# Optimization experiments

Measured on AMD Instinct MI355X. Metric: run time of the kernel, lower is better.

Reference implementation:

```python
import jax, jax.numpy as jnp
import numpy as np

N = 50000
E = 600000
D = 128


def gcn_conv(x, row, col, w, W, b):
    """PyG GCNConv: add self-loops (weight 1), symmetric deg^-1/2 normalization,
    linear transform, edge-weighted scatter-add aggregation, then bias."""
    n = x.shape[0]
    loop = jnp.arange(n)
    r = jnp.concatenate([row, loop])            # source nodes, [E+N]
    c = jnp.concatenate([col, loop])            # target nodes, [E+N]
    ww = jnp.concatenate([w, jnp.ones((n,), x.dtype)])
    deg = jax.ops.segment_sum(ww, c, num_segments=n)          # weighted in-degree
    dinv = jnp.where(deg > 0, jax.lax.rsqrt(deg), jnp.zeros_like(deg))
    norm = dinv[r] * ww * dinv[c]               # [E+N]
    xl = x @ W                                  # [n, D_out]
    msg = norm[:, None] * xl[r]                 # gather + scale, [E+N, D_out]
    out = jax.ops.segment_sum(msg, c, num_segments=n)
    return out + b


def setup_inputs() -> dict:
    key = jax.random.key(0)
    ks = jax.random.split(key, 12)
    x = jax.random.normal(ks[0], (N, D), dtype=jnp.float32)
    edge_index = jax.random.randint(ks[1], (2, E), 0, N, dtype=jnp.int64)
    edge_weights = jax.random.uniform(ks[2], (E,), dtype=jnp.float32)
    s = 1.0 / np.sqrt(D)
    W1 = jax.random.uniform(ks[3], (D, D), jnp.float32, -s, s)
    b1 = jnp.zeros((D,), jnp.float32)
    W2 = jax.random.uniform(ks[4], (D, D), jnp.float32, -s, s)
    b2 = jnp.zeros((D,), jnp.float32)
    W3 = jax.random.uniform(ks[5], (D, D), jnp.float32, -s, s)
    b3 = jnp.zeros((D,), jnp.float32)
    prelu_w = jnp.array(0.25, jnp.float32)
    return {"x": x, "edge_index": edge_index, "edge_weights": edge_weights,
            "W1": W1, "b1": b1, "W2": W2, "b2": b2, "W3": W3, "b3": b3,
            "prelu_w": prelu_w}


def reference(x, edge_index, edge_weights, W1, b1, W2, b2, W3, b3, prelu_w):
    row, col = edge_index[0], edge_index[1]
    # layer 1: GCNConv -> (dropout: eval, identity) -> ELU
    h = gcn_conv(x, row, col, edge_weights, W1, b1)
    h = jax.nn.elu(h)
    # layer 2: GCNConv -> GELU (torch default = exact erf)
    h = gcn_conv(h, row, col, edge_weights, W2, b2)
    h = jax.nn.gelu(h, approximate=False)
    # layer 3: GCNConv -> PReLU (learnable scalar slope)
    h = gcn_conv(h, row, col, edge_weights, W3, b3)
    h = jnp.where(h >= 0, h, prelu_w * h)
    return h
```

## Files before the change

### kernel.cpp

```cpp
#include <hip/hip_runtime.h>
#include <hip/hip_fp16.h>
#include <math.h>

constexpr int D = 128;

struct __align__(16) H8 { __half2 h[4]; };
struct __align__(8)  H4 { __half2 a, b; };


__device__ __forceinline__ int detect64(const int* __restrict__ ei) {
  int z = 0;
#pragma unroll
  for (int i = 0; i < 8; ++i) z |= ei[2 * i + 1];
  return (z == 0) ? 1 : 0;
}

__device__ __forceinline__ void load_edge(const int* __restrict__ ei, int e, int nE,
                                          int m64, int n, int& r, int& c) {
  if (m64) { r = ei[2 * (size_t)e]; c = ei[2 * ((size_t)nE + e)]; }
  else     { r = ei[(size_t)e];     c = ei[(size_t)nE + e]; }
  r = min(max(r, 0), n - 1);
  c = min(max(c, 0), n - 1);
}

__global__ void k_zero(int* __restrict__ cnt, int n) {
  int i = blockIdx.x * blockDim.x + threadIdx.x;
  if (i < n) cnt[i] = 0;
}

__global__ void k_pos(const int* __restrict__ ei, int* __restrict__ cnt,
                      int2* __restrict__ rc, int* __restrict__ pos, int nE, int n) {
  int e = blockIdx.x * blockDim.x + threadIdx.x;
  if (e >= nE) return;
  int m64 = detect64(ei);
  int r, c;
  load_edge(ei, e, nE, m64, n, r, c);
  rc[e] = make_int2(r, c);
  pos[e] = atomicAdd(&cnt[c], 1);
}

__global__ void k_scan1(const int* __restrict__ cnt, int* __restrict__ offs,
                        int* __restrict__ bsum, int n) {
  __shared__ int s[256];
  int t = threadIdx.x;
  int i = blockIdx.x * 256 + t;
  int v = (i < n) ? cnt[i] : 0;
  s[t] = v;
  __syncthreads();
  for (int off = 1; off < 256; off <<= 1) {
    int x = 0;
    if (t >= off) x = s[t - off];
    __syncthreads();
    if (t >= off) s[t] += x;
    __syncthreads();
  }
  if (i < n) offs[i] = s[t] - v;
  if (t == 255) bsum[blockIdx.x] = s[255];
}

__global__ void k_scan2(const int* __restrict__ bsum, int* __restrict__ boff, int nb) {
  __shared__ int s[256];
  int t = threadIdx.x;
  int v = (t < nb) ? bsum[t] : 0;
  s[t] = v;
  __syncthreads();
  for (int off = 1; off < 256; off <<= 1) {
    int x = 0;
    if (t >= off) x = s[t - off];
    __syncthreads();
    if (t >= off) s[t] += x;
    __syncthreads();
  }
  if (t < nb) boff[t] = s[t] - v;
}

__global__ void k_scan3(int* __restrict__ offs, const int* __restrict__ boff, int n, int nE) {
  int i = blockIdx.x * 256 + threadIdx.x;
  if (i < n) offs[i] += boff[blockIdx.x];
  if (i == 0) offs[n] = nE;
}

__global__ void k_fill(const int2* __restrict__ rc, const int* __restrict__ pos,
                       const float* __restrict__ w, const int* __restrict__ offs,
                       int2* __restrict__ ecf, int nE) {
  int e = blockIdx.x * blockDim.x + threadIdx.x;
  if (e >= nE) return;
  int2 p = rc[e];
  int idx = offs[p.y] + pos[e];
  ecf[idx] = make_int2(p.x, __float_as_int(w[e]));
}

__global__ void k_degdinv(const int2* __restrict__ ecf, const int* __restrict__ offs,
                          float* __restrict__ dinv, int n) {
  int i = blockIdx.x * blockDim.x + threadIdx.x;
  if (i >= n) return;
  float s = 1.0f;
  int e1 = offs[i + 1];
  for (int e = offs[i]; e < e1; ++e) s += __int_as_float(ecf[e].y);
  dinv[i] = rsqrtf(s);
}

template <int ACT>
__device__ __forceinline__ float act_f(float x) {
  if (ACT == 1) return x > 0.f ? x : expm1f(x);
  if (ACT == 2) return 0.5f * x * (1.0f + erff(x * 0.70710678118654752440f));
  return x;
}

template <int ACT, typename AT>
__global__ __launch_bounds__(256, 2) void k_gemm(const AT* __restrict__ A,
                                                 const float* __restrict__ W,
                                                 __half* __restrict__ Y, int n) {
  __shared__ float As[128 * 33];
  __shared__ float Ws[32 * 128];
  const int tid = threadIdx.x;
  const int row0 = blockIdx.x * 128;
  const int tc = tid & 15;
  const int tr = tid >> 4;

  float acc[8][8];
#pragma unroll
  for (int i = 0; i < 8; ++i)
#pragma unroll
    for (int j = 0; j < 8; ++j) acc[i][j] = 0.f;

  for (int kt = 0; kt < 4; ++kt) {
    if constexpr (sizeof(AT) == 4) {
#pragma unroll
      for (int i = 0; i < 4; ++i) {
        int idx = tid + i * 256;
        int r = idx >> 3;
        int c4 = idx & 7;
        float4 v = make_float4(0.f, 0.f, 0.f, 0.f);
        int gr = row0 + r;
        if (gr < n) v = *(const float4*)((const float*)A + (size_t)gr * D + kt * 32 + c4 * 4);
        As[r * 33 + c4 * 4 + 0] = act_f<ACT>(v.x);
        As[r * 33 + c4 * 4 + 1] = act_f<ACT>(v.y);
        As[r * 33 + c4 * 4 + 2] = act_f<ACT>(v.z);
        As[r * 33 + c4 * 4 + 3] = act_f<ACT>(v.w);
      }
    } else {
#pragma unroll
      for (int i = 0; i < 2; ++i) {
        int idx = tid + i * 256;
        int r = idx >> 2;
        int c8 = idx & 3;
        float f[8] = {0.f, 0.f, 0.f, 0.f, 0.f, 0.f, 0.f, 0.f};
        int gr = row0 + r;
        if (gr < n) {
          H8 v = *(const H8*)((const __half*)A + (size_t)gr * D + kt * 32 + c8 * 8);
#pragma unroll
          for (int t = 0; t < 4; ++t) {
            float2 p = __half22float2(v.h[t]);
            f[2 * t] = p.x; f[2 * t + 1] = p.y;
          }
        }
#pragma unroll
        for (int t = 0; t < 8; ++t)
          As[r * 33 + c8 * 8 + t] = act_f<ACT>(f[t]);
      }
    }
#pragma unroll
    for (int i = 0; i < 4; ++i) {
      int idx = tid + i * 256;
      int r = idx >> 5;
      int c4 = idx & 31;
      *(float4*)(&Ws[r * 128 + c4 * 4]) =
          *(const float4*)(W + (size_t)(kt * 32 + r) * D + c4 * 4);
    }
    __syncthreads();
#pragma unroll
    for (int k = 0; k < 32; ++k) {
      float a[8];
#pragma unroll
      for (int i = 0; i < 8; ++i) a[i] = As[(tr * 8 + i) * 33 + k];
      const float4 b0 = *(const float4*)(&Ws[k * 128 + tc * 4]);
      const float4 b1 = *(const float4*)(&Ws[k * 128 + tc * 4 + 64]);
#pragma unroll
      for (int i = 0; i < 8; ++i) {
        acc[i][0] += a[i] * b0.x; acc[i][1] += a[i] * b0.y;
        acc[i][2] += a[i] * b0.z; acc[i][3] += a[i] * b0.w;
        acc[i][4] += a[i] * b1.x; acc[i][5] += a[i] * b1.y;
        acc[i][6] += a[i] * b1.z; acc[i][7] += a[i] * b1.w;
      }
    }
    __syncthreads();
  }
#pragma unroll
  for (int i = 0; i < 8; ++i) {
    int gr = row0 + tr * 8 + i;
    if (gr < n) {
      H4 lo, hi;
      lo.a = __floats2half2_rn(acc[i][0], acc[i][1]);
      lo.b = __floats2half2_rn(acc[i][2], acc[i][3]);
      hi.a = __floats2half2_rn(acc[i][4], acc[i][5]);
      hi.b = __floats2half2_rn(acc[i][6], acc[i][7]);
      *(H4*)(Y + (size_t)gr * D + tc * 4) = lo;
      *(H4*)(Y + (size_t)gr * D + tc * 4 + 64) = hi;
    }
  }
}

__device__ __forceinline__ void fmacc8(float* acc, float c, const H8& y) {
  float2 f;
  f = __half22float2(y.h[0]); acc[0] += c * f.x; acc[1] += c * f.y;
  f = __half22float2(y.h[1]); acc[2] += c * f.x; acc[3] += c * f.y;
  f = __half22float2(y.h[2]); acc[4] += c * f.x; acc[5] += c * f.y;
  f = __half22float2(y.h[3]); acc[6] += c * f.x; acc[7] += c * f.y;
}

template <int PRELU, typename OutT>
__global__ __launch_bounds__(256) void k_agg(const __half* __restrict__ Y,
                                             const int* __restrict__ offs,
                                             const int2* __restrict__ ecf,
                                             const float* __restrict__ dinv,
                                             const float* __restrict__ bias,
                                             const float* __restrict__ pw,
                                             OutT* __restrict__ OUT, int n) {
  int gi = blockIdx.x * blockDim.x + threadIdx.x;
  int node = gi >> 5;
  int sub = (gi >> 4) & 1;
  int j = gi & 15;
  if (node >= n) return;
  float dc = dinv[node];
  float acc[8] = {0.f, 0.f, 0.f, 0.f, 0.f, 0.f, 0.f, 0.f};
  if (sub == 0) {
    H8 ys = *(const H8*)(Y + (size_t)node * D + j * 8);
    fmacc8(acc, dc, ys);
  }
  int e0 = offs[node], e1 = offs[node + 1];
  int e = e0 + sub;
  for (; e + 6 < e1; e += 8) {
    int2 p0 = ecf[e], p1 = ecf[e + 2], p2 = ecf[e + 4], p3 = ecf[e + 6];
    float c0 = dinv[p0.x] * __int_as_float(p0.y);
    float c1 = dinv[p1.x] * __int_as_float(p1.y);
    float c2 = dinv[p2.x] * __int_as_float(p2.y);
    float c3 = dinv[p3.x] * __int_as_float(p3.y);
    H8 y0 = *(const H8*)(Y + (size_t)p0.x * D + j * 8);
    H8 y1 = *(const H8*)(Y + (size_t)p1.x * D + j * 8);
    H8 y2 = *(const H8*)(Y + (size_t)p2.x * D + j * 8);
    H8 y3 = *(const H8*)(Y + (size_t)p3.x * D + j * 8);
    fmacc8(acc, c0, y0);
    fmacc8(acc, c1, y1);
    fmacc8(acc, c2, y2);
    fmacc8(acc, c3, y3);
  }
  for (; e < e1; e += 2) {
    int2 p = ecf[e];
    float c = dinv[p.x] * __int_as_float(p.y);
    H8 y = *(const H8*)(Y + (size_t)p.x * D + j * 8);
    fmacc8(acc, c, y);
  }
#pragma unroll
  for (int i = 0; i < 8; ++i) acc[i] += __shfl_xor(acc[i], 16, 64);
  float4 b4 = *(const float4*)(bias + j * 8 + sub * 4);
  float o[4];
  o[0] = dc * acc[sub * 4 + 0] + b4.x;
  o[1] = dc * acc[sub * 4 + 1] + b4.y;
  o[2] = dc * acc[sub * 4 + 2] + b4.z;
  o[3] = dc * acc[sub * 4 + 3] + b4.w;
  if (PRELU) {
    float wv = *pw;
#pragma unroll
    for (int i = 0; i < 4; ++i) o[i] = o[i] >= 0.f ? o[i] : wv * o[i];
  }
  if constexpr (sizeof(OutT) == 4) {
    *(float4*)((float*)OUT + (size_t)node * D + j * 8 + sub * 4) =
        make_float4(o[0], o[1], o[2], o[3]);
  } else {
    H4 hv;
    hv.a = __floats2half2_rn(o[0], o[1]);
    hv.b = __floats2half2_rn(o[2], o[3]);
    *(H4*)((__half*)OUT + (size_t)node * D + j * 8 + sub * 4) = hv;
  }
}

extern "C" void kernel_launch(void* const* d_in, const int* in_sizes, int n_in,
                              void* d_out, int out_size, void* d_ws, size_t ws_size,
                              hipStream_t stream) {
  const float* x  = (const float*)d_in[0];
  const int*   ei = (const int*)d_in[1];
  const float* w  = (const float*)d_in[2];
  const float* W1 = (const float*)d_in[3];
  const float* b1 = (const float*)d_in[4];
  const float* W2 = (const float*)d_in[5];
  const float* b2 = (const float*)d_in[6];
  const float* W3 = (const float*)d_in[7];
  const float* b3 = (const float*)d_in[8];
  const float* pw = (const float*)d_in[9];
  const int N = in_sizes[0] / D;
  const int E = in_sizes[2];
  float* out = (float*)d_out;

  char* wsb = (char*)d_ws;
  size_t off = 0;
  auto alloc = [&](size_t bytes) {
    void* p = wsb + off;
    off = (off + bytes + 255) & ~(size_t)255;
    return p;
  };
  float*  dinv = (float*)alloc((size_t)N * 4);
  int*    cnt  = (int*)alloc((size_t)N * 4);
  int*    offs = (int*)alloc((size_t)(N + 1) * 4);
  int*    bsum = (int*)alloc(256 * 4);
  int*    boff = (int*)alloc(256 * 4);
  int2*   ecf  = (int2*)alloc((size_t)E * 8);
  __half* Y    = (__half*)alloc((size_t)N * D * 2);
  __half* h    = (__half*)alloc((size_t)N * D * 2);
  int2*   rc   = (int2*)Y;
  int*    pos  = (int*)((char*)Y + (size_t)E * 8);

  const int nb = (N + 255) / 256;
  const int eb = (E + 255) / 256;

  hipLaunchKernelGGL(k_zero,    dim3(nb), dim3(256), 0, stream, cnt, N);
  hipLaunchKernelGGL(k_pos,     dim3(eb), dim3(256), 0, stream, ei, cnt, rc, pos, E, N);
  hipLaunchKernelGGL(k_scan1,   dim3(nb), dim3(256), 0, stream, cnt, offs, bsum, N);
  hipLaunchKernelGGL(k_scan2,   dim3(1),  dim3(256), 0, stream, bsum, boff, nb);
  hipLaunchKernelGGL(k_scan3,   dim3(nb), dim3(256), 0, stream, offs, boff, N, E);
  hipLaunchKernelGGL(k_fill,    dim3(eb), dim3(256), 0, stream, rc, pos, w, offs, ecf, E);
  hipLaunchKernelGGL(k_degdinv, dim3(nb), dim3(256), 0, stream, ecf, offs, dinv, N);

  const int gb = (N + 127) / 128;
  const int ab = (N * 32 + 255) / 256;

  hipLaunchKernelGGL((k_gemm<0, float>),  dim3(gb), dim3(256), 0, stream, x, W1, Y, N);
  hipLaunchKernelGGL((k_agg<0, __half>),  dim3(ab), dim3(256), 0, stream, Y, offs, ecf, dinv, b1, pw, h, N);
  hipLaunchKernelGGL((k_gemm<1, __half>), dim3(gb), dim3(256), 0, stream, h, W2, Y, N);
  hipLaunchKernelGGL((k_agg<0, __half>),  dim3(ab), dim3(256), 0, stream, Y, offs, ecf, dinv, b2, pw, h, N);
  hipLaunchKernelGGL((k_gemm<2, __half>), dim3(gb), dim3(256), 0, stream, h, W3, Y, N);
  hipLaunchKernelGGL((k_agg<1, float>),   dim3(ab), dim3(256), 0, stream, Y, offs, ecf, dinv, b3, pw, out, N);
}
```

Before: 323.5 us.

## Use column-chunked feature layout and packed fp16 edge coefficients in aggregation

```diff
diff --git a/kernel.cpp b/kernel.cpp
--- a/kernel.cpp
+++ b/kernel.cpp
@@ -98,6 +98,16 @@
   int e1 = offs[i + 1];
   for (int e = offs[i]; e < e1; ++e) s += __int_as_float(ecf[e].y);
   dinv[i] = rsqrtf(s);
+}
+
+__global__ void k_coef(const int2* __restrict__ ecf, const float* __restrict__ dinv,
+                       unsigned int* __restrict__ ecf2, int nE) {
+  int e = blockIdx.x * blockDim.x + threadIdx.x;
+  if (e >= nE) return;
+  int2 p = ecf[e];
+  float c = dinv[p.x] * __int_as_float(p.y);
+  ecf2[e] = ((unsigned int)p.x << 16) |
+            (unsigned int)__half_as_ushort(__float2half_rn(c));
 }
 
 template <int ACT>
@@ -143,12 +153,12 @@
 #pragma unroll
       for (int i = 0; i < 2; ++i) {
         int idx = tid + i * 256;
-        int r = idx >> 2;
-        int c8 = idx & 3;
+        int jcl = idx >> 7;
+        int r = idx & 127;
         float f[8] = {0.f, 0.f, 0.f, 0.f, 0.f, 0.f, 0.f, 0.f};
         int gr = row0 + r;
         if (gr < n) {
-          H8 v = *(const H8*)((const __half*)A + (size_t)gr * D + kt * 32 + c8 * 8);
+          H8 v = *(const H8*)((const __half*)A + ((size_t)(kt * 4 + jcl) * n + gr) * 8);
 #pragma unroll
           for (int t = 0; t < 4; ++t) {
             float2 p = __half22float2(v.h[t]);
@@ -157,7 +167,7 @@
         }
 #pragma unroll
         for (int t = 0; t < 8; ++t)
-          As[r * 33 + c8 * 8 + t] = act_f<ACT>(f[t]);
+          As[r * 33 + jcl * 8 + t] = act_f<ACT>(f[t]);
       }
     }
 #pragma unroll
@@ -186,6 +196,8 @@
     }
     __syncthreads();
   }
+  const int jc0 = tc >> 1;
+  const int off0 = (tc & 1) * 4;
 #pragma unroll
   for (int i = 0; i < 8; ++i) {
     int gr = row0 + tr * 8 + i;
@@ -195,8 +207,8 @@
       lo.b = __floats2half2_rn(acc[i][2], acc[i][3]);
       hi.a = __floats2half2_rn(acc[i][4], acc[i][5]);
       hi.b = __floats2half2_rn(acc[i][6], acc[i][7]);
-      *(H4*)(Y + (size_t)gr * D + tc * 4) = lo;
-      *(H4*)(Y + (size_t)gr * D + tc * 4 + 64) = hi;
+      *(H4*)(Y + ((size_t)jc0 * n + gr) * 8 + off0) = lo;
+      *(H4*)(Y + ((size_t)(8 + jc0) * n + gr) * 8 + off0) = hi;
     }
   }
 }
@@ -209,69 +221,68 @@
   f = __half22float2(y.h[3]); acc[6] += c * f.x; acc[7] += c * f.y;
 }
 
+__device__ __forceinline__ float cdecode(unsigned int u) {
+  return __half2float(__ushort_as_half((unsigned short)(u & 0xffffu)));
+}
+
 template <int PRELU, typename OutT>
 __global__ __launch_bounds__(256) void k_agg(const __half* __restrict__ Y,
                                              const int* __restrict__ offs,
-                                             const int2* __restrict__ ecf,
+                                             const unsigned int* __restrict__ ecf2,
                                              const float* __restrict__ dinv,
                                              const float* __restrict__ bias,
                                              const float* __restrict__ pw,
                                              OutT* __restrict__ OUT, int n) {
-  int gi = blockIdx.x * blockDim.x + threadIdx.x;
-  int node = gi >> 5;
-  int sub = (gi >> 4) & 1;
-  int j = gi & 15;
+  const int jc = blockIdx.x & 15;
+  const int node = (blockIdx.x >> 4) * 256 + threadIdx.x;
   if (node >= n) return;
+  const __half* Yj = Y + (size_t)jc * n * 8;
   float dc = dinv[node];
   float acc[8] = {0.f, 0.f, 0.f, 0.f, 0.f, 0.f, 0.f, 0.f};
-  if (sub == 0) {
-    H8 ys = *(const H8*)(Y + (size_t)node * D + j * 8);
+  {
+    H8 ys = *(const H8*)(Yj + (size_t)node * 8);
     fmacc8(acc, dc, ys);
   }
   int e0 = offs[node], e1 = offs[node + 1];
-  int e = e0 + sub;
-  for (; e + 6 < e1; e += 8) {
-    int2 p0 = ecf[e], p1 = ecf[e + 2], p2 = ecf[e + 4], p3 = ecf[e + 6];
-    float c0 = dinv[p0.x] * __int_as_float(p0.y);
-    float c1 = dinv[p1.x] * __int_as_float(p1.y);
-    float c2 = dinv[p2.x] * __int_as_float(p2.y);
-    float c3 = dinv[p3.x] * __int_as_float(p3.y);
-    H8 y0 = *(const H8*)(Y + (size_t)p0.x * D + j * 8);
-    H8 y1 = *(const H8*)(Y + (size_t)p1.x * D + j * 8);
-    H8 y2 = *(const H8*)(Y + (size_t)p2.x * D + j * 8);
-    H8 y3 = *(const H8*)(Y + (size_t)p3.x * D + j * 8);
-    fmacc8(acc, c0, y0);
-    fmacc8(acc, c1, y1);
-    fmacc8(acc, c2, y2);
-    fmacc8(acc, c3, y3);
-  }
-  for (; e < e1; e += 2) {
-    int2 p = ecf[e];
-    float c = dinv[p.x] * __int_as_float(p.y);
-    H8 y = *(const H8*)(Y + (size_t)p.x * D + j * 8);
-    fmacc8(acc, c, y);
-  }
-#pragma unroll
-  for (int i = 0; i < 8; ++i) acc[i] += __shfl_xor(acc[i], 16, 64);
-  float4 b4 = *(const float4*)(bias + j * 8 + sub * 4);
-  float o[4];
-  o[0] = dc * acc[sub * 4 + 0] + b4.x;
-  o[1] = dc * acc[sub * 4 + 1] + b4.y;
-  o[2] = dc * acc[sub * 4 + 2] + b4.z;
-  o[3] = dc * acc[sub * 4 + 3] + b4.w;
+  int e = e0;
+  for (; e + 4 <= e1; e += 4) {
+    unsigned int u0 = ecf2[e], u1 = ecf2[e + 1], u2 = ecf2[e + 2], u3 = ecf2[e + 3];
+    H8 y0 = *(const H8*)(Yj + (size_t)(u0 >> 16) * 8);
+    H8 y1 = *(const H8*)(Yj + (size_t)(u1 >> 16) * 8);
+    H8 y2 = *(const H8*)(Yj + (size_t)(u2 >> 16) * 8);
+    H8 y3 = *(const H8*)(Yj + (size_t)(u3 >> 16) * 8);
+    fmacc8(acc, cdecode(u0), y0);
+    fmacc8(acc, cdecode(u1), y1);
+    fmacc8(acc, cdecode(u2), y2);
+    fmacc8(acc, cdecode(u3), y3);
+  }
+  for (; e < e1; ++e) {
+    unsigned int u = ecf2[e];
+    H8 y = *(const H8*)(Yj + (size_t)(u >> 16) * 8);
+    fmacc8(acc, cdecode(u), y);
+  }
+  float4 b0 = *(const float4*)(bias + jc * 8);
+  float4 b1 = *(const float4*)(bias + jc * 8 + 4);
+  float o[8];
+  o[0] = dc * acc[0] + b0.x; o[1] = dc * acc[1] + b0.y;
+  o[2] = dc * acc[2] + b0.z; o[3] = dc * acc[3] + b0.w;
+  o[4] = dc * acc[4] + b1.x; o[5] = dc * acc[5] + b1.y;
+  o[6] = dc * acc[6] + b1.z; o[7] = dc * acc[7] + b1.w;
   if (PRELU) {
     float wv = *pw;
 #pragma unroll
-    for (int i = 0; i < 4; ++i) o[i] = o[i] >= 0.f ? o[i] : wv * o[i];
-  }
-  if constexpr (sizeof(OutT) == 4) {
-    *(float4*)((float*)OUT + (size_t)node * D + j * 8 + sub * 4) =
-        make_float4(o[0], o[1], o[2], o[3]);
+    for (int i = 0; i < 8; ++i) o[i] = o[i] >= 0.f ? o[i] : wv * o[i];
+  }
+  if constexpr (sizeof(OutT) == 2) {
+    H8 hv;
+    hv.h[0] = __floats2half2_rn(o[0], o[1]);
+    hv.h[1] = __floats2half2_rn(o[2], o[3]);
+    hv.h[2] = __floats2half2_rn(o[4], o[5]);
+    hv.h[3] = __floats2half2_rn(o[6], o[7]);
+    *(H8*)((__half*)OUT + ((size_t)jc * n + node) * 8) = hv;
   } else {
-    H4 hv;
-    hv.a = __floats2half2_rn(o[0], o[1]);
-    hv.b = __floats2half2_rn(o[2], o[3]);
-    *(H4*)((__half*)OUT + (size_t)node * D + j * 8 + sub * 4) = hv;
+    *(float4*)((float*)OUT + (size_t)node * D + jc * 8)     = make_float4(o[0], o[1], o[2], o[3]);
+    *(float4*)((float*)OUT + (size_t)node * D + jc * 8 + 4) = make_float4(o[4], o[5], o[6], o[7]);
   }
 }
 
@@ -299,16 +310,17 @@
     off = (off + bytes + 255) & ~(size_t)255;
     return p;
   };
-  float*  dinv = (float*)alloc((size_t)N * 4);
-  int*    cnt  = (int*)alloc((size_t)N * 4);
-  int*    offs = (int*)alloc((size_t)(N + 1) * 4);
-  int*    bsum = (int*)alloc(256 * 4);
-  int*    boff = (int*)alloc(256 * 4);
-  int2*   ecf  = (int2*)alloc((size_t)E * 8);
-  __half* Y    = (__half*)alloc((size_t)N * D * 2);
-  __half* h    = (__half*)alloc((size_t)N * D * 2);
-  int2*   rc   = (int2*)Y;
-  int*    pos  = (int*)((char*)Y + (size_t)E * 8);
+  float*        dinv = (float*)alloc((size_t)N * 4);
+  int*          cnt  = (int*)alloc((size_t)N * 4);
+  int*          offs = (int*)alloc((size_t)(N + 1) * 4);
+  int*          bsum = (int*)alloc(256 * 4);
+  int*          boff = (int*)alloc(256 * 4);
+  int2*         ecf  = (int2*)alloc((size_t)E * 8);
+  unsigned int* ecf2 = (unsigned int*)alloc((size_t)E * 4);
+  __half*       Y    = (__half*)alloc((size_t)N * D * 2);
+  __half*       h    = (__half*)alloc((size_t)N * D * 2);
+  int2*         rc   = (int2*)Y;
+  int*          pos  = (int*)((char*)Y + (size_t)E * 8);
 
   const int nb = (N + 255) / 256;
   const int eb = (E + 255) / 256;
@@ -320,14 +332,15 @@
   hipLaunchKernelGGL(k_scan3,   dim3(nb), dim3(256), 0, stream, offs, boff, N, E);
   hipLaunchKernelGGL(k_fill,    dim3(eb), dim3(256), 0, stream, rc, pos, w, offs, ecf, E);
   hipLaunchKernelGGL(k_degdinv, dim3(nb), dim3(256), 0, stream, ecf, offs, dinv, N);
+  hipLaunchKernelGGL(k_coef,    dim3(eb), dim3(256), 0, stream, ecf, dinv, ecf2, E);
 
   const int gb = (N + 127) / 128;
-  const int ab = (N * 32 + 255) / 256;
+  const int ab = 16 * ((N + 255) / 256);
 
   hipLaunchKernelGGL((k_gemm<0, float>),  dim3(gb), dim3(256), 0, stream, x, W1, Y, N);
-  hipLaunchKernelGGL((k_agg<0, __half>),  dim3(ab), dim3(256), 0, stream, Y, offs, ecf, dinv, b1, pw, h, N);
+  hipLaunchKernelGGL((k_agg<0, __half>),  dim3(ab), dim3(256), 0, stream, Y, offs, ecf2, dinv, b1, pw, h, N);
   hipLaunchKernelGGL((k_gemm<1, __half>), dim3(gb), dim3(256), 0, stream, h, W2, Y, N);
-  hipLaunchKernelGGL((k_agg<0, __half>),  dim3(ab), dim3(256), 0, stream, Y, offs, ecf, dinv, b2, pw, h, N);
+  hipLaunchKernelGGL((k_agg<0, __half>),  dim3(ab), dim3(256), 0, stream, Y, offs, ecf2, dinv, b2, pw, h, N);
   hipLaunchKernelGGL((k_gemm<2, __half>), dim3(gb), dim3(256), 0, stream, h, W3, Y, N);
-  hipLaunchKernelGGL((k_agg<1, float>),   dim3(ab), dim3(256), 0, stream, Y, offs, ecf, dinv, b3, pw, out, N);
-}
+  hipLaunchKernelGGL((k_agg<1, float>),   dim3(ab), dim3(256), 0, stream, Y, offs, ecf2, dinv, b3, pw, out, N);
+}
```

Result: slower. 407.4 us (+26.0%).
